# Performance work log

Hardware: AMD Instinct MI355X
Metric: run time of the kernel (lower is better)

## Reference

```python
import jax, jax.numpy as jnp
import numpy as np

NUM_CLASSES = 2
TOP_K = 200
CONF_THRESH = 0.01
NMS_THRESH = 0.45
VAR0, VAR1 = 0.1, 0.2
NUM_PRIORS = 72192
BATCH = 64


def setup_inputs() -> dict:
    key = jax.random.key(0)
    k1, k2, k3 = jax.random.split(key, 3)
    loc_data = jax.random.normal(k1, (BATCH, NUM_PRIORS, 4), dtype=jnp.float32)
    conf_data = jax.random.uniform(k2, (BATCH * NUM_PRIORS, NUM_CLASSES), dtype=jnp.float32)
    prior_data = jax.random.uniform(k3, (NUM_PRIORS, 4), dtype=jnp.float32) * 0.5 + 0.01
    return {"loc_data": loc_data, "conf_data": conf_data, "prior_data": prior_data}


def decode(loc, priors):
    # loc, priors: [P, 4] (cx, cy, w, h) -> corners (x1, y1, x2, y2)
    cxcy = priors[:, :2] + loc[:, :2] * VAR0 * priors[:, 2:]
    wh = priors[:, 2:] * jnp.exp(loc[:, 2:] * VAR1)
    return jnp.concatenate([cxcy - wh / 2, cxcy + wh / 2], axis=-1)


def pairwise_iou(boxes):
    # boxes: [K, 4] corners
    area = (boxes[:, 2] - boxes[:, 0]) * (boxes[:, 3] - boxes[:, 1])
    lt = jnp.maximum(boxes[:, None, :2], boxes[None, :, :2])
    rb = jnp.minimum(boxes[:, None, 2:], boxes[None, :, 2:])
    wh = jnp.clip(rb - lt, 0.0)
    inter = wh[..., 0] * wh[..., 1]
    union = area[:, None] + area[None, :] - inter
    return inter / jnp.maximum(union, 1e-12)


def nms_single(boxes, scores):
    # boxes: [P,4], scores: [P] -> [TOP_K, 5] rows (score, x1, y1, x2, y2)
    masked = jnp.where(scores > CONF_THRESH, scores, -jnp.inf)
    top_scores, idx = jax.lax.top_k(masked, TOP_K)      # descending, like torch nms
    cand_boxes = boxes[idx]                              # [K,4]
    valid = top_scores > CONF_THRESH
    iou = pairwise_iou(cand_boxes)                       # [K,K]
    ar = jnp.arange(TOP_K)

    def body(i, keep):
        sup = (iou[i] > NMS_THRESH) & (ar > i)
        return jnp.where(keep[i], keep & ~sup, keep)

    keep = jax.lax.fori_loop(0, TOP_K, body, valid)
    # compact kept detections to the front (matches output[i, cl, :count] = ...)
    pos = jnp.cumsum(keep) - 1
    pos = jnp.where(keep, pos, TOP_K)                    # dropped rows scatter out of range
    rows = jnp.concatenate([top_scores[:, None], cand_boxes], axis=1)
    return jnp.zeros((TOP_K, 5), dtype=boxes.dtype).at[pos].set(rows, mode="drop")


def reference(loc_data, conf_data, prior_data):
    num = loc_data.shape[0]
    num_priors = prior_data.shape[0]
    conf_preds = conf_data.reshape(num, num_priors, NUM_CLASSES)  # [B, P, C]
    decoded = jax.vmap(decode, in_axes=(0, None))(loc_data, prior_data)  # [B, P, 4]
    per_class = []
    # class 0 is background -> zeros (matches torch output init)
    per_class.append(jnp.zeros((num, TOP_K, 5), dtype=loc_data.dtype))
    for cl in range(1, NUM_CLASSES):
        per_class.append(jax.vmap(nms_single)(decoded, conf_preds[:, :, cl]))
    # final rank-based zeroing in torch source is a no-op (fill_ on an advanced-index copy)
    return jnp.stack(per_class, axis=1)  # [B, C, TOP_K, 5]
```

## Files before the change

kernel.cpp:

```cpp
#include <hip/hip_runtime.h>
#include <math.h>

#pragma clang fp contract(off)

#define NUM_PRIORS 72192
#define BATCH      64
#define TOPK       200
#define CONF_TH    0.01f
#define NMS_TH     0.45f
#define NBINS      256
#define SLICES     32
#define ROWS       (NUM_PRIORS / SLICES)
#define Q4         (ROWS / 2)
#define QB         (NUM_PRIORS / 2)
#define CAPS       64
#define CAP        1024
#define KW         7
#define NMS_NTH    1024
#define B255       0.99609375f

typedef unsigned long long u64;

__device__ __forceinline__ int bin_of(float s) {
    int b = (int)(s * 256.0f);
    return b > 255 ? 255 : b;
}

__global__ __launch_bounds__(256) void collect255_kernel(const float* __restrict__ conf,
                                                         unsigned* __restrict__ scnt,
                                                         u64* __restrict__ cand) {
    __shared__ unsigned lcnt;
    const int b = blockIdx.y, slice = blockIdx.x, tid = threadIdx.x;
    if (tid == 0) lcnt = 0;
    __syncthreads();
    const float4* c4 = (const float4*)conf;
    const long base4 = (long)b * QB + (long)slice * Q4;
    const int prow0 = slice * ROWS;
    u64* seg = cand + ((long)b * SLICES + slice) * CAPS;

    float4 v0 = c4[base4 + tid];
    float4 v1 = c4[base4 + tid + 256];
    float4 v2 = c4[base4 + tid + 512];
    float4 v3 = c4[base4 + tid + 768];

#define P255(sv, pidx)                                                          \
    do {                                                                        \
        float s_ = (sv);                                                        \
        if (s_ >= B255) {                                                       \
            unsigned pos = atomicAdd(&lcnt, 1u);                                \
            if (pos < CAPS)                                                     \
                seg[pos] = ((u64)__float_as_uint(s_) << 32) |                   \
                           (u64)(0xFFFFFFFFu - (unsigned)(pidx));               \
        }                                                                       \
    } while (0)

    P255(v0.y, prow0 + 2 * tid);
    P255(v0.w, prow0 + 2 * tid + 1);
    P255(v1.y, prow0 + 2 * (tid + 256));
    P255(v1.w, prow0 + 2 * (tid + 256) + 1);
    P255(v2.y, prow0 + 2 * (tid + 512));
    P255(v2.w, prow0 + 2 * (tid + 512) + 1);
    P255(v3.y, prow0 + 2 * (tid + 768));
    P255(v3.w, prow0 + 2 * (tid + 768) + 1);
    if (tid < Q4 - 1024) {
        float4 vt = c4[base4 + tid + 1024];
        P255(vt.y, prow0 + 2 * (tid + 1024));
        P255(vt.w, prow0 + 2 * (tid + 1024) + 1);
    }
#undef P255
    __syncthreads();
    if (tid == 0) scnt[b * SLICES + slice] = lcnt;
}

__global__ __launch_bounds__(NMS_NTH) void nms_kernel(const float* __restrict__ loc,
                           const float* __restrict__ prior,
                           const float* __restrict__ conf,
                           const unsigned* __restrict__ scnt,
                           u64* __restrict__ cand,
                           float* __restrict__ out) {
    __shared__ u64 keys[CAP];
    __shared__ float4 bbox[224];
    __shared__ float bsc_s[TOPK];
    __shared__ unsigned invR[TOPK][8];
    __shared__ unsigned kw0[8];
    __shared__ unsigned kwF[KW];
    __shared__ int soff[SLICES + 1];
    __shared__ int scl[SLICES];
    __shared__ unsigned histc[NBINS];
    __shared__ unsigned lcnt32[SLICES];
    __shared__ int TshC, needfix;
    const int b = blockIdx.x, tid = threadIdx.x;

    if (tid < 64) {
        int s = tid;
        unsigned cs = (s < SLICES) ? scnt[b * SLICES + s] : 0u;
        int c = (cs < CAPS) ? (int)cs : CAPS;
        int v = c;
#pragma unroll
        for (int d = 1; d < 32; d <<= 1) {
            int o = __shfl_up(v, d);
            if ((int)tid >= d) v += o;
        }
        unsigned tot = cs;
#pragma unroll
        for (int d = 32; d >= 1; d >>= 1) tot += __shfl_xor(tot, d);
        u64 ovb = __ballot(cs > CAPS);
        if (s < SLICES) {
            int P = v - c;
            int off = P > CAP ? CAP : P;
            int rem = CAP - off;
            int cl = c < rem ? c : rem;
            soff[s] = off;
            scl[s] = cl;
            if (s == SLICES - 1) soff[SLICES] = (P + c > CAP) ? CAP : (P + c);
        }
        if (tid == 0) {
            needfix = (tot < TOPK) || (ovb != 0ull);
            TshC = 0;
        }
    }
    {
        float* ob = out + (long)b * 2 * TOPK * 5;
        for (int i = tid; i < 2 * TOPK * 5; i += NMS_NTH) ob[i] = 0.f;
    }
    if (tid < 8) kw0[tid] = 0u;
    __syncthreads();

    if (needfix) {
        const float4* c4 = (const float4*)conf;
        for (int i = tid; i < NBINS; i += NMS_NTH) histc[i] = 0u;
        __syncthreads();
        for (int q = tid; q < QB; q += NMS_NTH) {
            float4 v = c4[(long)b * QB + q];
            if (v.y > CONF_TH) atomicAdd(&histc[bin_of(v.y)], 1u);
            if (v.w > CONF_TH) atomicAdd(&histc[bin_of(v.w)], 1u);
        }
        __syncthreads();
        for (int off = 1; off < NBINS; off <<= 1) {
            unsigned vv = 0u;
            if (tid < NBINS && tid + off < NBINS) vv = histc[tid + off];
            __syncthreads();
            if (tid < NBINS) histc[tid] += vv;
            __syncthreads();
        }
        if (tid < NBINS) {
            unsigned s0 = histc[tid];
            unsigned sn = (tid + 1 < NBINS) ? histc[tid + 1] : 0u;
            if (s0 >= TOPK && (tid == NBINS - 1 || sn < TOPK)) TshC = tid;
        }
        if (tid < SLICES) lcnt32[tid] = 0u;
        __syncthreads();
        const int T = TshC;
        for (int q = tid; q < QB; q += NMS_NTH) {
            float4 v = c4[(long)b * QB + q];
            int sl = q / Q4;
            u64* seg = cand + ((long)b * SLICES + sl) * CAPS;
            if (v.y > CONF_TH && bin_of(v.y) >= T) {
                unsigned pos = atomicAdd(&lcnt32[sl], 1u);
                if (pos < CAPS)
                    seg[pos] = ((u64)__float_as_uint(v.y) << 32) |
                               (u64)(0xFFFFFFFFu - (unsigned)(2 * q));
            }
            if (v.w > CONF_TH && bin_of(v.w) >= T) {
                unsigned pos = atomicAdd(&lcnt32[sl], 1u);
                if (pos < CAPS)
                    seg[pos] = ((u64)__float_as_uint(v.w) << 32) |
                               (u64)(0xFFFFFFFFu - (unsigned)(2 * q + 1));
            }
        }
        __syncthreads();
        if (tid < 64) {
            int s = tid;
            unsigned cs = (s < SLICES) ? lcnt32[s] : 0u;
            int c = (cs < CAPS) ? (int)cs : CAPS;
            int v = c;
#pragma unroll
            for (int d = 1; d < 32; d <<= 1) {
                int o = __shfl_up(v, d);
                if ((int)tid >= d) v += o;
            }
            if (s < SLICES) {
                int P = v - c;
                int off = P > CAP ? CAP : P;
                int rem = CAP - off;
                int cl = c < rem ? c : rem;
                soff[s] = off;
                scl[s] = cl;
                if (s == SLICES - 1) soff[SLICES] = (P + c > CAP) ? CAP : (P + c);
            }
        }
        __syncthreads();
    }

    const int n = soff[SLICES];
    const int nn = (n + 15) & ~15;
    for (int pos = tid; pos < SLICES * CAPS; pos += NMS_NTH) {
        int s = pos >> 6, idx = pos & 63;
        if (idx < scl[s])
            keys[soff[s] + idx] = cand[((long)b * SLICES + s) * CAPS + idx];
    }
    for (int i = n + tid; i < nn; i += NMS_NTH) keys[i] = 0ull;
    __syncthreads();

    u64 kc = (tid < n) ? keys[tid] : 0ull;
    int rk = 0;
    if ((int)(tid & ~63u) < n) {
        for (int k = 0; k < nn; k += 16) {
            u64 kb[16];
#pragma unroll
            for (int j = 0; j < 16; j++) kb[j] = keys[k + j];
#pragma unroll
            for (int j = 0; j < 16; j++) rk += (kb[j] > kc) ? 1 : 0;
        }
    }
    if (tid < n && rk < TOPK) {
        u64 key = kc;
        float sc = __uint_as_float((unsigned)(key >> 32));
        unsigned p = 0xFFFFFFFFu - (unsigned)(key & 0xFFFFFFFFull);
        float4 l4 = ((const float4*)loc)[(long)b * NUM_PRIORS + p];
        float4 p4 = ((const float4*)prior)[p];
        float cx = p4.x + (l4.x * 0.1f) * p4.z;
        float cy = p4.y + (l4.y * 0.1f) * p4.w;
        float w_ = p4.z * (float)exp((double)(l4.z * 0.2f));
        float h_ = p4.w * (float)exp((double)(l4.w * 0.2f));
        float x1 = cx - w_ * 0.5f, y1 = cy - h_ * 0.5f;
        float x2 = cx + w_ * 0.5f, y2 = cy + h_ * 0.5f;
        bsc_s[rk] = sc;
        bbox[rk] = make_float4(x1, y1, x2, y2);
        atomicOr(&kw0[rk >> 5], 1u << (rk & 31));
    }
    __syncthreads();

    {
        const int q = tid >> 8, i = tid & 255;
        if (i < TOPK) {
            const float4 ib = bbox[i];
            const float iar = (ib.z - ib.x) * (ib.w - ib.y);
#pragma unroll
            for (int wi = 0; wi < 2; wi++) {
                if (wi == 1 && q == 3) break;
                const int w = (wi == 0) ? q : q + 4;
                const int jbase = w * 32;
                unsigned inv = 0xFFFFFFFFu;
#pragma unroll
                for (int g = 0; g < 32; g += 8) {
                    float4 J[8];
#pragma unroll
                    for (int r = 0; r < 8; r++) J[r] = bbox[jbase + g + r];
#pragma unroll
                    for (int r = 0; r < 8; r++) {
                        const int j = jbase + g + r;
                        if (j > i && j < TOPK) {
                            float4 jb = J[r];
                            float jar = (jb.z - jb.x) * (jb.w - jb.y);
                            float ltx = fmaxf(ib.x, jb.x);
                            float lty = fmaxf(ib.y, jb.y);
                            float rbx = fminf(ib.z, jb.z);
                            float rby = fminf(ib.w, jb.w);
                            float wx = fmaxf(rbx - ltx, 0.0f);
                            float wy = fmaxf(rby - lty, 0.0f);
                            float inter = wx * wy;
                            float uni = (iar + jar) - inter;
                            float iou = inter / fmaxf(uni, 1e-12f);
                            if (iou > NMS_TH) inv &= ~(1u << (g + r));
                        }
                    }
                }
                invR[i][w] = inv;
            }
        }
    }
    __syncthreads();

    if (tid < 64) {
        unsigned kk[KW];
#pragma unroll
        for (int w = 0; w < KW; w++) kk[w] = kw0[w];
#pragma unroll
        for (int g = 0; g < TOPK; g += 8) {
            uint4 A[8], C[8];
#pragma unroll
            for (int r = 0; r < 8; r++) {
                A[r] = *(const uint4*)&invR[g + r][0];
                C[r] = *(const uint4*)&invR[g + r][4];
            }
#pragma unroll
            for (int r = 0; r < 8; r++) {
                const int i = g + r;
                if ((kk[i >> 5] >> (i & 31)) & 1u) {
                    kk[0] &= A[r].x; kk[1] &= A[r].y; kk[2] &= A[r].z; kk[3] &= A[r].w;
                    kk[4] &= C[r].x; kk[5] &= C[r].y; kk[6] &= C[r].z;
                }
            }
        }
        if (tid == 0) {
            kwF[0] = kk[0]; kwF[1] = kk[1]; kwF[2] = kk[2]; kwF[3] = kk[3];
            kwF[4] = kk[4]; kwF[5] = kk[5]; kwF[6] = kk[6];
        }
    }
    __syncthreads();

    if (tid < TOPK) {
        const int wsel = tid >> 5, bsel = tid & 31;
        if ((kwF[wsel] >> bsel) & 1u) {
            int pos = 0;
#pragma unroll
            for (int w = 0; w < KW; w++) {
                unsigned kw_ = kwF[w];
                if (w < wsel) pos += __popc(kw_);
                else if (w == wsel) pos += __popc(kw_ & ((bsel == 0) ? 0u : (0xFFFFFFFFu >> (32 - bsel))));
            }
            float4 jb = bbox[tid];
            float* o = out + (((long)b * 2 + 1) * TOPK + pos) * 5;
            o[0] = bsc_s[tid];
            o[1] = jb.x;
            o[2] = jb.y;
            o[3] = jb.z;
            o[4] = jb.w;
        }
    }
}

extern "C" void kernel_launch(void* const* d_in, const int* in_sizes, int n_in,
                              void* d_out, int out_size, void* d_ws, size_t ws_size,
                              hipStream_t stream) {
    const float* loc   = (const float*)d_in[0];
    const float* conf  = (const float*)d_in[1];
    const float* prior = (const float*)d_in[2];
    float* out = (float*)d_out;

    char* w = (char*)d_ws;
    unsigned* scnt = (unsigned*)w;
    u64* cand      = (u64*)(w + 8192);

    collect255_kernel<<<dim3(SLICES, BATCH), 256, 0, stream>>>(conf, scnt, cand);
    nms_kernel<<<BATCH, NMS_NTH, 0, stream>>>(loc, prior, conf, scnt, cand, out);
}
```

Baseline: 38.75 us.

## Split NMS kernel into 256-thread rank/decode and 1024-thread IoU/greedy kernels

Divides the monolithic per-batch NMS kernel in two. The first runs 256 threads per image, each ranking four candidate keys and writing the decoded top boxes, scores and keep bitmask to workspace. The second loads these, builds the IoU suppression matrix with 1024 threads and runs the greedy pass. The greedy loop now skips 8-row groups with no live bits. The split targets lighter per-phase resource use and less idle-thread waste, at the cost of an extra launch and a global-memory round trip.

Measured after the change: 48.85 us. 26.1% more time.

```diff
diff --git a/kernel.cpp b/kernel.cpp
--- a/kernel.cpp
+++ b/kernel.cpp
@@ -16,7 +16,6 @@
 #define CAPS       64
 #define CAP        1024
 #define KW         7
-#define NMS_NTH    1024
 #define B255       0.99609375f
 
 typedef unsigned long long u64;
@@ -72,18 +71,16 @@
     if (tid == 0) scnt[b * SLICES + slice] = lcnt;
 }
 
-__global__ __launch_bounds__(NMS_NTH) void nms_kernel(const float* __restrict__ loc,
+__global__ __launch_bounds__(256) void rankdecode_kernel(const float* __restrict__ loc,
                            const float* __restrict__ prior,
                            const float* __restrict__ conf,
                            const unsigned* __restrict__ scnt,
                            u64* __restrict__ cand,
+                           float4* __restrict__ gbox,
+                           float* __restrict__ gsc,
+                           unsigned* __restrict__ gkw,
                            float* __restrict__ out) {
     __shared__ u64 keys[CAP];
-    __shared__ float4 bbox[224];
-    __shared__ float bsc_s[TOPK];
-    __shared__ unsigned invR[TOPK][8];
-    __shared__ unsigned kw0[8];
-    __shared__ unsigned kwF[KW];
     __shared__ int soff[SLICES + 1];
     __shared__ int scl[SLICES];
     __shared__ unsigned histc[NBINS];
@@ -119,18 +116,18 @@
             TshC = 0;
         }
     }
+    if (tid >= 64 && tid < 72) gkw[b * 8 + (tid - 64)] = 0u;
     {
         float* ob = out + (long)b * 2 * TOPK * 5;
-        for (int i = tid; i < 2 * TOPK * 5; i += NMS_NTH) ob[i] = 0.f;
-    }
-    if (tid < 8) kw0[tid] = 0u;
+        for (int i = tid; i < 2 * TOPK * 5; i += 256) ob[i] = 0.f;
+    }
     __syncthreads();
 
     if (needfix) {
         const float4* c4 = (const float4*)conf;
-        for (int i = tid; i < NBINS; i += NMS_NTH) histc[i] = 0u;
-        __syncthreads();
-        for (int q = tid; q < QB; q += NMS_NTH) {
+        for (int i = tid; i < NBINS; i += 256) histc[i] = 0u;
+        __syncthreads();
+        for (int q = tid; q < QB; q += 256) {
             float4 v = c4[(long)b * QB + q];
             if (v.y > CONF_TH) atomicAdd(&histc[bin_of(v.y)], 1u);
             if (v.w > CONF_TH) atomicAdd(&histc[bin_of(v.w)], 1u);
@@ -151,7 +148,7 @@
         if (tid < SLICES) lcnt32[tid] = 0u;
         __syncthreads();
         const int T = TshC;
-        for (int q = tid; q < QB; q += NMS_NTH) {
+        for (int q = tid; q < QB; q += 256) {
             float4 v = c4[(long)b * QB + q];
             int sl = q / Q4;
             u64* seg = cand + ((long)b * SLICES + sl) * CAPS;
@@ -194,41 +191,82 @@
 
     const int n = soff[SLICES];
     const int nn = (n + 15) & ~15;
-    for (int pos = tid; pos < SLICES * CAPS; pos += NMS_NTH) {
+    for (int pos = tid; pos < SLICES * CAPS; pos += 256) {
         int s = pos >> 6, idx = pos & 63;
         if (idx < scl[s])
             keys[soff[s] + idx] = cand[((long)b * SLICES + s) * CAPS + idx];
     }
-    for (int i = n + tid; i < nn; i += NMS_NTH) keys[i] = 0ull;
-    __syncthreads();
-
-    u64 kc = (tid < n) ? keys[tid] : 0ull;
-    int rk = 0;
-    if ((int)(tid & ~63u) < n) {
-        for (int k = 0; k < nn; k += 16) {
-            u64 kb[16];
-#pragma unroll
-            for (int j = 0; j < 16; j++) kb[j] = keys[k + j];
-#pragma unroll
-            for (int j = 0; j < 16; j++) rk += (kb[j] > kc) ? 1 : 0;
-        }
-    }
-    if (tid < n && rk < TOPK) {
-        u64 key = kc;
-        float sc = __uint_as_float((unsigned)(key >> 32));
-        unsigned p = 0xFFFFFFFFu - (unsigned)(key & 0xFFFFFFFFull);
-        float4 l4 = ((const float4*)loc)[(long)b * NUM_PRIORS + p];
-        float4 p4 = ((const float4*)prior)[p];
-        float cx = p4.x + (l4.x * 0.1f) * p4.z;
-        float cy = p4.y + (l4.y * 0.1f) * p4.w;
-        float w_ = p4.z * (float)exp((double)(l4.z * 0.2f));
-        float h_ = p4.w * (float)exp((double)(l4.w * 0.2f));
-        float x1 = cx - w_ * 0.5f, y1 = cy - h_ * 0.5f;
-        float x2 = cx + w_ * 0.5f, y2 = cy + h_ * 0.5f;
-        bsc_s[rk] = sc;
-        bbox[rk] = make_float4(x1, y1, x2, y2);
-        atomicOr(&kw0[rk >> 5], 1u << (rk & 31));
-    }
+    for (int i = n + tid; i < nn; i += 256) keys[i] = 0ull;
+    __syncthreads();
+
+    const int smax = (n + 255) >> 8;
+    u64 kc0 = (tid < n) ? keys[tid] : 0ull;
+    u64 kc1 = (tid + 256 < n) ? keys[tid + 256] : 0ull;
+    u64 kc2 = (tid + 512 < n) ? keys[tid + 512] : 0ull;
+    u64 kc3 = (tid + 768 < n) ? keys[tid + 768] : 0ull;
+    int r0 = 0, r1 = 0, r2 = 0, r3 = 0;
+    for (int k = 0; k < nn; k += 16) {
+        u64 kb[16];
+#pragma unroll
+        for (int j = 0; j < 16; j++) kb[j] = keys[k + j];
+        if (smax > 0) {
+#pragma unroll
+            for (int j = 0; j < 16; j++) r0 += (kb[j] > kc0) ? 1 : 0;
+        }
+        if (smax > 1) {
+#pragma unroll
+            for (int j = 0; j < 16; j++) r1 += (kb[j] > kc1) ? 1 : 0;
+        }
+        if (smax > 2) {
+#pragma unroll
+            for (int j = 0; j < 16; j++) r2 += (kb[j] > kc2) ? 1 : 0;
+        }
+        if (smax > 3) {
+#pragma unroll
+            for (int j = 0; j < 16; j++) r3 += (kb[j] > kc3) ? 1 : 0;
+        }
+    }
+#define DECODE(cidx, key, r)                                                    \
+    do {                                                                        \
+        if ((cidx) < n && (r) < TOPK) {                                         \
+            float sc = __uint_as_float((unsigned)((key) >> 32));                \
+            unsigned p = 0xFFFFFFFFu - (unsigned)((key) & 0xFFFFFFFFull);       \
+            float4 l4 = ((const float4*)loc)[(long)b * NUM_PRIORS + p];         \
+            float4 p4 = ((const float4*)prior)[p];                              \
+            float cx = p4.x + (l4.x * 0.1f) * p4.z;                             \
+            float cy = p4.y + (l4.y * 0.1f) * p4.w;                             \
+            float w_ = p4.z * (float)exp((double)(l4.z * 0.2f));                \
+            float h_ = p4.w * (float)exp((double)(l4.w * 0.2f));                \
+            float x1 = cx - w_ * 0.5f, y1 = cy - h_ * 0.5f;                     \
+            float x2 = cx + w_ * 0.5f, y2 = cy + h_ * 0.5f;                     \
+            gbox[(long)b * TOPK + (r)] = make_float4(x1, y1, x2, y2);           \
+            gsc[(long)b * TOPK + (r)] = sc;                                     \
+            atomicOr(&gkw[b * 8 + ((r) >> 5)], 1u << ((r) & 31));               \
+        }                                                                       \
+    } while (0)
+    DECODE(tid, kc0, r0);
+    DECODE(tid + 256, kc1, r1);
+    DECODE(tid + 512, kc2, r2);
+    DECODE(tid + 768, kc3, r3);
+#undef DECODE
+}
+
+__global__ __launch_bounds__(1024) void invrgreedy_kernel(const float4* __restrict__ gbox,
+                           const float* __restrict__ gsc,
+                           const unsigned* __restrict__ gkw,
+                           float* __restrict__ out) {
+    __shared__ float4 bbox[224];
+    __shared__ float bsc_s[TOPK];
+    __shared__ unsigned invR[TOPK][8];
+    __shared__ unsigned kw0[8];
+    __shared__ unsigned kwF[KW];
+    const int b = blockIdx.x, tid = threadIdx.x;
+
+    if (tid < 224)
+        bbox[tid] = (tid < TOPK) ? gbox[(long)b * TOPK + tid]
+                                 : make_float4(0.f, 0.f, 0.f, 0.f);
+    if (tid >= 256 && tid < 256 + TOPK) bsc_s[tid - 256] = gsc[(long)b * TOPK + (tid - 256)];
+    if (tid >= 480 && tid < 488) kw0[tid - 480] = gkw[b * 8 + (tid - 480)];
     __syncthreads();
 
     {
@@ -278,6 +316,8 @@
         for (int w = 0; w < KW; w++) kk[w] = kw0[w];
 #pragma unroll
         for (int g = 0; g < TOPK; g += 8) {
+            const unsigned live = (kk[g >> 5] >> (g & 31)) & 0xFFu;
+            if (live == 0u) continue;
             uint4 A[8], C[8];
 #pragma unroll
             for (int r = 0; r < 8; r++) {
@@ -332,7 +372,12 @@
     char* w = (char*)d_ws;
     unsigned* scnt = (unsigned*)w;
     u64* cand      = (u64*)(w + 8192);
+    float4* gbox   = (float4*)(w + 1056768);
+    float* gsc     = (float*)(w + 1261568);
+    unsigned* gkw  = (unsigned*)(w + 1312768);
 
     collect255_kernel<<<dim3(SLICES, BATCH), 256, 0, stream>>>(conf, scnt, cand);
-    nms_kernel<<<BATCH, NMS_NTH, 0, stream>>>(loc, prior, conf, scnt, cand, out);
-}
+    rankdecode_kernel<<<BATCH, 256, 0, stream>>>(loc, prior, conf, scnt, cand,
+                                                 gbox, gsc, gkw, out);
+    invrgreedy_kernel<<<BATCH, 1024, 0, stream>>>(gbox, gsc, gkw, out);
+}
```
